# Kernel optimization log

Measured on AMD Instinct MI355X. Metric: run time of the kernel, lower is better.

## Reference

```python
import jax, jax.numpy as jnp
import numpy as np

N_NODES = 100000
N_EDGES = 1200000
D_IN = 64
D_OUT = 64


def setup_inputs() -> dict:
    key = jax.random.key(0)
    ks = jax.random.split(key, 8)
    feat = jax.random.normal(ks[0], (N_NODES, D_IN), dtype=jnp.float32)
    src = jax.random.randint(ks[1], (N_EDGES,), 0, N_NODES, dtype=jnp.int32)
    dst = jax.random.randint(ks[2], (N_EDGES,), 0, N_NODES, dtype=jnp.int32)
    edge_weight = jax.random.uniform(ks[3], (N_EDGES, 1), dtype=jnp.float32)
    edge_mask = jax.random.uniform(ks[4], (N_EDGES, 1), dtype=jnp.float32)
    W_self = jax.random.normal(ks[5], (D_OUT, D_IN), dtype=jnp.float32) * (1.0 / np.sqrt(D_IN))
    b_self = jnp.zeros((D_OUT,), dtype=jnp.float32)
    W_neigh = jax.random.normal(ks[6], (D_OUT, D_IN), dtype=jnp.float32) * (1.0 / np.sqrt(D_IN))
    b_neigh = jnp.zeros((D_OUT,), dtype=jnp.float32)
    return {"feat": feat, "src": src, "dst": dst, "edge_weight": edge_weight,
            "edge_mask": edge_mask, "W_self": W_self, "b_self": b_self,
            "W_neigh": W_neigh, "b_neigh": b_neigh}


def reference(feat, src, dst, edge_weight, edge_mask, W_self, b_self, W_neigh, b_neigh):
    # message: gather src feats, scale by per-edge weight and mask  -> [E, D_IN]
    msg = feat[src] * edge_weight * edge_mask
    # mean scatter-reduce over incoming edges per dst node
    neigh_sum = jax.ops.segment_sum(msg, dst, num_segments=N_NODES)  # [N, D_IN]
    deg = jax.ops.segment_sum(jnp.ones((msg.shape[0],), dtype=feat.dtype), dst,
                              num_segments=N_NODES)  # [N]
    h_neigh = neigh_sum / jnp.maximum(deg, 1.0)[:, None]  # zero-degree nodes -> 0 (DGL mean semantics)
    # dual linear fuse
    rst = (feat @ W_self.T + b_self) + (h_neigh @ W_neigh.T + b_neigh)
    return rst
```

## Files before the change

kernel.cpp:

```cpp
#include <hip/hip_runtime.h>

#define NB_MAX   1568
#define CAP      1024
#define BT_EDGES 5120
#define BT_TPB   1024
#define EPE      5

typedef __attribute__((ext_vector_type(4))) float floatx4;
typedef __attribute__((ext_vector_type(2))) float floatx2;
typedef __attribute__((ext_vector_type(8))) short bf16x8;
typedef __attribute__((ext_vector_type(4))) unsigned uintx4;

__device__ __forceinline__ unsigned short f32_to_bf16(float f) {
  unsigned u = __float_as_uint(f);
  u = (u + 0x7fffu + ((u >> 16) & 1u)) >> 16;
  return (unsigned short)u;
}
__device__ __forceinline__ unsigned pack2(float a, float b) {
  return (unsigned)f32_to_bf16(a) | ((unsigned)f32_to_bf16(b) << 16);
}
__device__ __forceinline__ bf16x8 zero_bf16x8() {
  bf16x8 v;
#pragma unroll
  for (int i = 0; i < 8; ++i) v[i] = 0;
  return v;
}

#if __has_builtin(__builtin_amdgcn_cvt_pk_fp8_f32)
__device__ __forceinline__ unsigned pack_fp8x4(float a, float b, float c, float d) {
  unsigned v = (unsigned)__builtin_amdgcn_cvt_pk_fp8_f32(a, b, 0, false);
  v = (unsigned)__builtin_amdgcn_cvt_pk_fp8_f32(c, d, (int)v, true);
  return v;
}
#else
__device__ __forceinline__ unsigned sw_f32_fp8(float f) {
  unsigned u = __float_as_uint(f);
  unsigned s = (u >> 24) & 0x80u;
  unsigned au = u & 0x7fffffffu;
  if (au > 0x43E00000u) au = 0x43E00000u;
  au += 0x7FFFFu + ((au >> 20) & 1u);
  int e = (int)(au >> 23) - 120;
  if (e <= 0) return s;
  return s | ((unsigned)e << 3) | ((au >> 20) & 7u);
}
__device__ __forceinline__ unsigned pack_fp8x4(float a, float b, float c, float d) {
  return sw_f32_fp8(a) | (sw_f32_fp8(b) << 8) | (sw_f32_fp8(c) << 16) |
         (sw_f32_fp8(d) << 24);
}
#endif

#if __has_builtin(__builtin_amdgcn_cvt_pk_f32_fp8)
__device__ __forceinline__ void dec4(float* acc, unsigned w32, float wt) {
  floatx2 f0 = __builtin_amdgcn_cvt_pk_f32_fp8((int)w32, false);
  floatx2 f1 = __builtin_amdgcn_cvt_pk_f32_fp8((int)w32, true);
  acc[0] += wt * f0.x; acc[1] += wt * f0.y;
  acc[2] += wt * f1.x; acc[3] += wt * f1.y;
}
#else
__device__ __forceinline__ float sw_fp8_f32(unsigned b) {
  unsigned s = (b & 0x80u) << 24;
  unsigned e = (b >> 3) & 0xFu;
  unsigned m = b & 7u;
  float fn = __uint_as_float(s | ((e + 120u) << 23) | (m << 20));
  float fd = (float)(int)m * 0.001953125f;
  fd = (b & 0x80u) ? -fd : fd;
  return e ? fn : fd;
}
__device__ __forceinline__ void dec4(float* acc, unsigned w32, float wt) {
  acc[0] += wt * sw_fp8_f32(w32 & 0xFF);
  acc[1] += wt * sw_fp8_f32((w32 >> 8) & 0xFF);
  acc[2] += wt * sw_fp8_f32((w32 >> 16) & 0xFF);
  acc[3] += wt * sw_fp8_f32(w32 >> 24);
}
#endif

__global__ __launch_bounds__(BT_TPB) void k_build(
    const float* __restrict__ feat, const int* __restrict__ src,
    const int* __restrict__ dst, const float* __restrict__ ew,
    const float* __restrict__ em, const float* __restrict__ Ws,
    const float* __restrict__ Wn, int* __restrict__ gCursor,
    unsigned* __restrict__ recs, unsigned short* __restrict__ featb,
    unsigned char* __restrict__ featq, unsigned short* __restrict__ Wb,
    int E, int nChunks, int nB) {
  __shared__ unsigned stage[BT_EDGES];
  __shared__ unsigned short stageB[BT_EDGES];
  __shared__ int A[NB_MAX];
  __shared__ int B[NB_MAX];
  __shared__ int waveSums[16];

  const int t = threadIdx.x;
  const int lane = t & 63;
  const int wvid = t >> 6;
  const int e0 = blockIdx.x * BT_EDGES;
  const int eEnd = min(e0 + BT_EDGES, E);
  const int nLocal = eEnd - e0;

  for (int i = t; i < NB_MAX; i += BT_TPB) B[i] = 0;
  __syncthreads();

  int dreg[EPE];
#pragma unroll
  for (int k = 0; k < EPE; ++k) {
    int i = e0 + k * BT_TPB + t;
    dreg[k] = -1;
    if (i < eEnd) {
      int d = __builtin_nontemporal_load(&dst[i]);
      dreg[k] = d;
      atomicAdd(&B[d >> 6], 1);
    }
  }
  __syncthreads();

  {
    const int EPT = 2;
    int b0 = t * EPT;
    int v[EPT];
    int sum = 0;
#pragma unroll
    for (int j = 0; j < EPT; ++j) {
      v[j] = (b0 + j < nB) ? B[b0 + j] : 0;
      sum += v[j];
    }
    int x = sum;
#pragma unroll
    for (int d = 1; d < 64; d <<= 1) {
      int y = __shfl_up(x, d, 64);
      if (lane >= d) x += y;
    }
    if (lane == 63) waveSums[wvid] = x;
    __syncthreads();
    int wprefix = 0;
    for (int i = 0; i < wvid; ++i) wprefix += waveSums[i];
    int run = wprefix + x - sum;
#pragma unroll
    for (int j = 0; j < EPT; ++j) {
      if (b0 + j < nB) A[b0 + j] = run;
      run += v[j];
    }
  }
  __syncthreads();

  for (int i = t; i < nB; i += BT_TPB) {
    int c = B[i];
    int l = A[i];
    int g = c ? atomicAdd(&gCursor[i], c) : 0;
    A[i] = i * CAP + g - l;
    B[i] = l;
  }
  __syncthreads();

#pragma unroll
  for (int k = 0; k < EPE; ++k) {
    int i = e0 + k * BT_TPB + t;
    if (i < eEnd) {
      int d = dreg[k];
      int bkt = d >> 6;
      int r = atomicAdd(&B[bkt], 1);
      float w = __builtin_nontemporal_load(&ew[i]) *
                __builtin_nontemporal_load(&em[i]);
      int wq = (int)(w * 511.0f + 0.5f);
      if (wq > 511) wq = 511;
      stage[r] = (unsigned)__builtin_nontemporal_load(&src[i]) |
                 ((unsigned)(d & 63) << 17) | ((unsigned)wq << 23);
      stageB[r] = (unsigned short)bkt;
    }
  }
  __syncthreads();

  for (int i = t; i < nLocal; i += BT_TPB) {
    int bkt = stageB[i];
    int pos = A[bkt] + i;
    if (pos < (bkt + 1) * CAP)
      recs[pos] = stage[i];
  }

  for (int c = blockIdx.x * BT_TPB + t; c < nChunks; c += gridDim.x * BT_TPB) {
    const floatx4* fp = reinterpret_cast<const floatx4*>(feat) + (size_t)c * 2;
    floatx4 a = __builtin_nontemporal_load(fp);
    floatx4 b = __builtin_nontemporal_load(fp + 1);
    uintx4 o;
    o.x = pack2(a.x, a.y);
    o.y = pack2(a.z, a.w);
    o.z = pack2(b.x, b.y);
    o.w = pack2(b.z, b.w);
    __builtin_nontemporal_store(o, reinterpret_cast<uintx4*>(featb) + c);
    uint2 q8;
    q8.x = pack_fp8x4(a.x, a.y, a.z, a.w);
    q8.y = pack_fp8x4(b.x, b.y, b.z, b.w);
    reinterpret_cast<uint2*>(featq)[c] = q8;
  }

  if (blockIdx.x == 0) {
    for (int i = t; i < 1024; i += BT_TPB) {
      int j = i >> 4, c4 = i & 15;
      float4 w4 = reinterpret_cast<const float4*>(Ws)[i];
      float4 n4 = reinterpret_cast<const float4*>(Wn)[i];
      *reinterpret_cast<uint2*>(&Wb[j * 128 + c4 * 4]) =
          make_uint2(pack2(w4.x, w4.y), pack2(w4.z, w4.w));
      *reinterpret_cast<uint2*>(&Wb[j * 128 + 64 + c4 * 4]) =
          make_uint2(pack2(n4.x, n4.y), pack2(n4.z, n4.w));
    }
  }
}

__global__ __launch_bounds__(512) void sage_gather_gemm(
    const unsigned short* __restrict__ featb,
    const unsigned char* __restrict__ featq,
    const unsigned short* __restrict__ Wb, const int* __restrict__ gCursor,
    const unsigned* __restrict__ recs, const float* __restrict__ bs,
    const float* __restrict__ bn, float* __restrict__ out, int N) {
  __shared__ unsigned short An[64][72];
  __shared__ unsigned rawL[CAP];
  __shared__ unsigned srtL[CAP];
  __shared__ int cntS[64], offS[64], curS[64];

  const int t = threadIdx.x;
  const int b = blockIdx.x;
  const int n0 = b * 64;
  const int base = b * CAP;
  const int cb = min(gCursor[b], CAP);

  if (t < 64) cntS[t] = 0;
  __syncthreads();

  for (int i = t; i < cb; i += 512) {
    unsigned r = __builtin_nontemporal_load(&recs[base + i]);
    rawL[i] = r;
    atomicAdd(&cntS[(r >> 17) & 63], 1);
  }

  const int wv8 = t >> 6;
  const int ntile = wv8 & 3;
  const int jh = wv8 >> 2;
  const int ln = t & 63;
  const int col = ln & 15;
  const int quad = ln >> 4;
  const int gn = n0 + ntile * 16 + col;
  bf16x8 af0 = zero_bf16x8(), af1 = zero_bf16x8();
  if (gn < N) {
    af0 = __builtin_nontemporal_load(
        reinterpret_cast<const bf16x8*>(featb + (size_t)gn * 64 + quad * 8));
    af1 = __builtin_nontemporal_load(
        reinterpret_cast<const bf16x8*>(featb + (size_t)gn * 64 + 32 + quad * 8));
  }
  const float bb0 = bs[(jh * 2) * 16 + col] + bn[(jh * 2) * 16 + col];
  const float bb1 = bs[(jh * 2 + 1) * 16 + col] + bn[(jh * 2 + 1) * 16 + col];
  __syncthreads();

  if (t < 64) {
    int c = cntS[t];
    int x = c;
#pragma unroll
    for (int d = 1; d < 64; d <<= 1) {
      int y = __shfl_up(x, d, 64);
      if (t >= d) x += y;
    }
    offS[t] = x - c;
    curS[t] = x - c;
  }
  __syncthreads();

  for (int i = t; i < cb; i += 512) {
    unsigned r = rawL[i];
    int p = atomicAdd(&curS[(r >> 17) & 63], 1);
    srtL[p] = r;
  }
  __syncthreads();

  {
    const int nl = t >> 3;
    const int g  = (t >> 2) & 1;
    const int q  = t & 3;
    const int deg = cntS[nl], off = offS[nl];
    const int myN = (deg - g + 1) >> 1;
    float acc[16];
#pragma unroll
    for (int i = 0; i < 16; ++i) acc[i] = 0.f;
    const uint4* fq = reinterpret_cast<const uint4*>(featq);

    uint4 uC = {0, 0, 0, 0}, uN = {0, 0, 0, 0};
    float wC = 0.f, wN = 0.f;
    if (myN > 0) {
      unsigned r0 = srtL[off + g];
      uC = fq[(size_t)(r0 & 0x1FFFF) * 4 + q];
      wC = (float)(r0 >> 23) * (1.0f / 511.0f);
    }
    if (myN > 1) {
      unsigned r1 = srtL[off + g + 2];
      uN = fq[(size_t)(r1 & 0x1FFFF) * 4 + q];
      wN = (float)(r1 >> 23) * (1.0f / 511.0f);
    }
    for (int m = 0; m < myN; ++m) {
      uint4 u = uC;
      float w = wC;
      uC = uN; wC = wN;
      if (m + 2 < myN) {
        unsigned rn = srtL[off + g + 2 * (m + 2)];
        uN = fq[(size_t)(rn & 0x1FFFF) * 4 + q];
        wN = (float)(rn >> 23) * (1.0f / 511.0f);
      }
      dec4(acc + 0, u.x, w);
      dec4(acc + 4, u.y, w);
      dec4(acc + 8, u.z, w);
      dec4(acc + 12, u.w, w);
    }

#pragma unroll
    for (int i = 0; i < 16; ++i) acc[i] += __shfl_xor(acc[i], 4, 64);

    if (g == 0) {
      float inv = 1.0f / fmaxf((float)deg, 1.0f);
#pragma unroll
      for (int i = 0; i < 16; ++i) acc[i] *= inv;
      uint4 o0, o1;
      o0.x = pack2(acc[0], acc[1]);
      o0.y = pack2(acc[2], acc[3]);
      o0.z = pack2(acc[4], acc[5]);
      o0.w = pack2(acc[6], acc[7]);
      o1.x = pack2(acc[8], acc[9]);
      o1.y = pack2(acc[10], acc[11]);
      o1.z = pack2(acc[12], acc[13]);
      o1.w = pack2(acc[14], acc[15]);
      *reinterpret_cast<uint4*>(&An[nl][q * 16]) = o0;
      *reinterpret_cast<uint4*>(&An[nl][q * 16 + 8]) = o1;
    }
  }
  __syncthreads();

  floatx4 acc4[2];
  acc4[0] = (floatx4){bb0, bb0, bb0, bb0};
  acc4[1] = (floatx4){bb1, bb1, bb1, bb1};

#pragma unroll
  for (int kk = 0; kk < 4; ++kk) {
    bf16x8 af;
    if (kk == 0)      af = af0;
    else if (kk == 1) af = af1;
    else
      af = *reinterpret_cast<const bf16x8*>(
          &An[ntile * 16 + col][(kk - 2) * 32 + quad * 8]);
#pragma unroll
    for (int jj = 0; jj < 2; ++jj) {
      int jt = jh * 2 + jj;
      bf16x8 bf = *reinterpret_cast<const bf16x8*>(
          Wb + (jt * 16 + col) * 128 + kk * 32 + quad * 8);
      acc4[jj] = __builtin_amdgcn_mfma_f32_16x16x32_bf16(af, bf, acc4[jj], 0, 0, 0);
    }
  }

#pragma unroll
  for (int jj = 0; jj < 2; ++jj) {
    int jt = jh * 2 + jj;
#pragma unroll
    for (int r = 0; r < 4; ++r) {
      int m = quad * 4 + r;
      int g2 = n0 + ntile * 16 + m;
      if (g2 < N)
        __builtin_nontemporal_store(acc4[jj][r],
                                    &out[(size_t)g2 * 64 + jt * 16 + col]);
    }
  }
}

extern "C" void kernel_launch(void* const* d_in, const int* in_sizes, int n_in,
                              void* d_out, int out_size, void* d_ws, size_t ws_size,
                              hipStream_t stream) {
  const float* feat = (const float*)d_in[0];
  const int*   src  = (const int*)d_in[1];
  const int*   dst  = (const int*)d_in[2];
  const float* ew   = (const float*)d_in[3];
  const float* em   = (const float*)d_in[4];
  const float* Ws   = (const float*)d_in[5];
  const float* bs   = (const float*)d_in[6];
  const float* Wn   = (const float*)d_in[7];
  const float* bn   = (const float*)d_in[8];
  float* out = (float*)d_out;

  const int N = in_sizes[0] / 64;
  const int E = in_sizes[1];
  const int nB = (N + 63) / 64;

  unsigned short* featb = (unsigned short*)d_ws;
  unsigned char*  featq = (unsigned char*)(featb + (size_t)N * 64);
  unsigned short* Wb    = (unsigned short*)(featq + (size_t)N * 64);
  unsigned* recs   = (unsigned*)(Wb + 64 * 128);
  int*      gCursor = (int*)(recs + (size_t)NB_MAX * CAP);

  hipMemsetAsync(gCursor, 0, NB_MAX * sizeof(int), stream);

  int nChunks = N * 8;
  int gB = (E + BT_EDGES - 1) / BT_EDGES;

  k_build<<<gB, BT_TPB, 0, stream>>>(feat, src, dst, ew, em, Ws, Wn,
                                     gCursor, recs, featb, featq, Wb,
                                     E, nChunks, nB);
  sage_gather_gemm<<<nB, 512, 0, stream>>>(featb, featq, Wb, gCursor, recs,
                                           bs, bn, out, N);
}
```

Before: 159.1 us.

## Halve gather-GEMM block to 256 threads, one thread-quad per node

The fused gather+GEMM kernel drops from 512 to 256 threads per block with a launch bound asking for 8 blocks per CU. Each node's edges are now handled by a single group of 4 lanes instead of two groups split on even/odd edges, which removes the cross-group shuffle reduction. Each wave now computes all four output column tiles in the MFMA stage, and the self-feature operand load moves from before the sort into the GEMM loop. The aim is higher occupancy and less reduction overhead, at the cost of longer serial per-node edge loops and less latency hiding for the self-feature load.

```diff
diff --git a/kernel.cpp b/kernel.cpp
--- a/kernel.cpp
+++ b/kernel.cpp
@@ -203,7 +203,7 @@
   }
 }
 
-__global__ __launch_bounds__(512) void sage_gather_gemm(
+__global__ __launch_bounds__(256, 8) void sage_gather_gemm(
     const unsigned short* __restrict__ featb,
     const unsigned char* __restrict__ featq,
     const unsigned short* __restrict__ Wb, const int* __restrict__ gCursor,
@@ -223,28 +223,11 @@
   if (t < 64) cntS[t] = 0;
   __syncthreads();
 
-  for (int i = t; i < cb; i += 512) {
+  for (int i = t; i < cb; i += 256) {
     unsigned r = __builtin_nontemporal_load(&recs[base + i]);
     rawL[i] = r;
     atomicAdd(&cntS[(r >> 17) & 63], 1);
   }
-
-  const int wv8 = t >> 6;
-  const int ntile = wv8 & 3;
-  const int jh = wv8 >> 2;
-  const int ln = t & 63;
-  const int col = ln & 15;
-  const int quad = ln >> 4;
-  const int gn = n0 + ntile * 16 + col;
-  bf16x8 af0 = zero_bf16x8(), af1 = zero_bf16x8();
-  if (gn < N) {
-    af0 = __builtin_nontemporal_load(
-        reinterpret_cast<const bf16x8*>(featb + (size_t)gn * 64 + quad * 8));
-    af1 = __builtin_nontemporal_load(
-        reinterpret_cast<const bf16x8*>(featb + (size_t)gn * 64 + 32 + quad * 8));
-  }
-  const float bb0 = bs[(jh * 2) * 16 + col] + bn[(jh * 2) * 16 + col];
-  const float bb1 = bs[(jh * 2 + 1) * 16 + col] + bn[(jh * 2 + 1) * 16 + col];
   __syncthreads();
 
   if (t < 64) {
@@ -260,7 +243,7 @@
   }
   __syncthreads();
 
-  for (int i = t; i < cb; i += 512) {
+  for (int i = t; i < cb; i += 256) {
     unsigned r = rawL[i];
     int p = atomicAdd(&curS[(r >> 17) & 63], 1);
     srtL[p] = r;
@@ -268,11 +251,9 @@
   __syncthreads();
 
   {
-    const int nl = t >> 3;
-    const int g  = (t >> 2) & 1;
+    const int nl = t >> 2;
     const int q  = t & 3;
     const int deg = cntS[nl], off = offS[nl];
-    const int myN = (deg - g + 1) >> 1;
     float acc[16];
 #pragma unroll
     for (int i = 0; i < 16; ++i) acc[i] = 0.f;
@@ -280,22 +261,22 @@
 
     uint4 uC = {0, 0, 0, 0}, uN = {0, 0, 0, 0};
     float wC = 0.f, wN = 0.f;
-    if (myN > 0) {
-      unsigned r0 = srtL[off + g];
+    if (deg > 0) {
+      unsigned r0 = srtL[off];
       uC = fq[(size_t)(r0 & 0x1FFFF) * 4 + q];
       wC = (float)(r0 >> 23) * (1.0f / 511.0f);
     }
-    if (myN > 1) {
-      unsigned r1 = srtL[off + g + 2];
+    if (deg > 1) {
+      unsigned r1 = srtL[off + 1];
       uN = fq[(size_t)(r1 & 0x1FFFF) * 4 + q];
       wN = (float)(r1 >> 23) * (1.0f / 511.0f);
     }
-    for (int m = 0; m < myN; ++m) {
+    for (int m = 0; m < deg; ++m) {
       uint4 u = uC;
       float w = wC;
       uC = uN; wC = wN;
-      if (m + 2 < myN) {
-        unsigned rn = srtL[off + g + 2 * (m + 2)];
+      if (m + 2 < deg) {
+        unsigned rn = srtL[off + m + 2];
         uN = fq[(size_t)(rn & 0x1FFFF) * 4 + q];
         wN = (float)(rn >> 23) * (1.0f / 511.0f);
       }
@@ -305,58 +286,66 @@
       dec4(acc + 12, u.w, w);
     }
 
-#pragma unroll
-    for (int i = 0; i < 16; ++i) acc[i] += __shfl_xor(acc[i], 4, 64);
-
-    if (g == 0) {
-      float inv = 1.0f / fmaxf((float)deg, 1.0f);
-#pragma unroll
-      for (int i = 0; i < 16; ++i) acc[i] *= inv;
-      uint4 o0, o1;
-      o0.x = pack2(acc[0], acc[1]);
-      o0.y = pack2(acc[2], acc[3]);
-      o0.z = pack2(acc[4], acc[5]);
-      o0.w = pack2(acc[6], acc[7]);
-      o1.x = pack2(acc[8], acc[9]);
-      o1.y = pack2(acc[10], acc[11]);
-      o1.z = pack2(acc[12], acc[13]);
-      o1.w = pack2(acc[14], acc[15]);
-      *reinterpret_cast<uint4*>(&An[nl][q * 16]) = o0;
-      *reinterpret_cast<uint4*>(&An[nl][q * 16 + 8]) = o1;
-    }
-  }
-  __syncthreads();
-
-  floatx4 acc4[2];
-  acc4[0] = (floatx4){bb0, bb0, bb0, bb0};
-  acc4[1] = (floatx4){bb1, bb1, bb1, bb1};
+    float inv = 1.0f / fmaxf((float)deg, 1.0f);
+#pragma unroll
+    for (int i = 0; i < 16; ++i) acc[i] *= inv;
+    uint4 o0, o1;
+    o0.x = pack2(acc[0], acc[1]);
+    o0.y = pack2(acc[2], acc[3]);
+    o0.z = pack2(acc[4], acc[5]);
+    o0.w = pack2(acc[6], acc[7]);
+    o1.x = pack2(acc[8], acc[9]);
+    o1.y = pack2(acc[10], acc[11]);
+    o1.z = pack2(acc[12], acc[13]);
+    o1.w = pack2(acc[14], acc[15]);
+    *reinterpret_cast<uint4*>(&An[nl][q * 16]) = o0;
+    *reinterpret_cast<uint4*>(&An[nl][q * 16 + 8]) = o1;
+  }
+  __syncthreads();
+
+  const int wv = t >> 6;
+  const int ln = t & 63;
+  const int col = ln & 15;
+  const int quad = ln >> 4;
+  const int gn = n0 + wv * 16 + col;
+
+  floatx4 acc4[4];
+#pragma unroll
+  for (int jt = 0; jt < 4; ++jt) {
+    float bb = bs[jt * 16 + col] + bn[jt * 16 + col];
+    acc4[jt] = (floatx4){bb, bb, bb, bb};
+  }
 
 #pragma unroll
   for (int kk = 0; kk < 4; ++kk) {
     bf16x8 af;
-    if (kk == 0)      af = af0;
-    else if (kk == 1) af = af1;
-    else
+    if (kk < 2) {
+      if (gn < N) {
+        af = *reinterpret_cast<const bf16x8*>(featb + (size_t)gn * 64 +
+                                              kk * 32 + quad * 8);
+      } else {
+        af = zero_bf16x8();
+      }
+    } else {
       af = *reinterpret_cast<const bf16x8*>(
-          &An[ntile * 16 + col][(kk - 2) * 32 + quad * 8]);
-#pragma unroll
-    for (int jj = 0; jj < 2; ++jj) {
-      int jt = jh * 2 + jj;
+          &An[wv * 16 + col][(kk - 2) * 32 + quad * 8]);
+    }
+#pragma unroll
+    for (int jt = 0; jt < 4; ++jt) {
       bf16x8 bf = *reinterpret_cast<const bf16x8*>(
           Wb + (jt * 16 + col) * 128 + kk * 32 + quad * 8);
-      acc4[jj] = __builtin_amdgcn_mfma_f32_16x16x32_bf16(af, bf, acc4[jj], 0, 0, 0);
-    }
-  }
-
-#pragma unroll
-  for (int jj = 0; jj < 2; ++jj) {
-    int jt = jh * 2 + jj;
+      acc4[jt] = __builtin_amdgcn_mfma_f32_16x16x32_bf16(af, bf, acc4[jt], 0, 0, 0);
+    }
+  }
+
+#pragma unroll
+  for (int jt = 0; jt < 4; ++jt) {
 #pragma unroll
     for (int r = 0; r < 4; ++r) {
       int m = quad * 4 + r;
-      int g2 = n0 + ntile * 16 + m;
+      int g2 = n0 + wv * 16 + m;
       if (g2 < N)
-        __builtin_nontemporal_store(acc4[jj][r],
+        __builtin_nontemporal_store(acc4[jt][r],
                                     &out[(size_t)g2 * 64 + jt * 16 + col]);
     }
   }
@@ -394,6 +383,6 @@
   k_build<<<gB, BT_TPB, 0, stream>>>(feat, src, dst, ew, em, Ws, Wn,
                                      gCursor, recs, featb, featq, Wb,
                                      E, nChunks, nB);
-  sage_gather_gemm<<<nB, 512, 0, stream>>>(featb, featq, Wb, gCursor, recs,
+  sage_gather_gemm<<<nB, 256, 0, stream>>>(featb, featq, Wb, gCursor, recs,
                                            bs, bn, out, N);
 }
```

Result: faster. 155.5 us (-2.2%).
